# Performance work log

Measured on AMD Instinct MI355X. Metric: run time of the kernel, lower is better.

The kernel has to match this reference:

```python
import jax, jax.numpy as jnp
import numpy as np

N_NODES = 50000
N_EDGES = 400000
H = 64          # node hidden state dim (entities_dimensions['node'])
E_DIM = 8       # edge_params dim (message.extra_parameters)
MSG_HID = 128   # message-creation MLP hidden width
RD_HID = 128    # readout hidden width
T = 2           # message-passing steps


def setup_inputs() -> dict:
    key = jax.random.key(0)
    ks = jax.random.split(key, 12)
    def w(k, shape):
        return jax.random.normal(k, shape, dtype=jnp.float32) * 0.05
    return {
        "node_feats": jax.random.normal(ks[0], (N_NODES, H), dtype=jnp.float32),
        "edge_feats": jax.random.normal(ks[1], (N_EDGES, E_DIM), dtype=jnp.float32),
        "edge_src": jax.random.randint(ks[2], (N_EDGES,), 0, N_NODES),
        "edge_dst": jax.random.randint(ks[3], (N_EDGES,), 0, N_NODES),
        # message creation MLP: concat(hs_src, hs_dst, edge_params) -> relu -> H
        "W_msg1": w(ks[4], (2 * H + E_DIM, MSG_HID)),
        "b_msg1": jnp.zeros((MSG_HID,), jnp.float32),
        "W_msg2": w(ks[5], (MSG_HID, H)),
        "b_msg2": jnp.zeros((H,), jnp.float32),
        # GRU cell update (keras GRUCell convention, reset_after=False)
        "W_x": w(ks[6], (H, 3 * H)),
        "W_h": w(ks[7], (H, 3 * H)),
        "b_gru": jnp.zeros((3 * H,), jnp.float32),
        # readout MLP: H -> relu -> 1
        "W_r1": w(ks[8], (H, RD_HID)),
        "b_r1": jnp.zeros((RD_HID,), jnp.float32),
        "W_r2": w(ks[9], (RD_HID, 1)),
        "b_r2": jnp.zeros((1,), jnp.float32),
    }


def _gru_cell(h, x, W_x, W_h, b):
    # gates order: update (z), reset (r), candidate (h~) — keras convention
    gx = x @ W_x + b
    gh = h @ W_h
    xz, xr, xh = jnp.split(gx, 3, axis=-1)
    hz, hr, hh = jnp.split(gh, 3, axis=-1)
    z = jax.nn.sigmoid(xz + hz)
    r = jax.nn.sigmoid(xr + hr)
    hc = jnp.tanh(xh + r * hh)
    return z * h + (1.0 - z) * hc


def reference(node_feats, edge_feats, edge_src, edge_dst,
              W_msg1, b_msg1, W_msg2, b_msg2,
              W_x, W_h, b_gru, W_r1, b_r1, W_r2, b_r2):
    h = node_feats  # [N, H] hidden states initialized from entity features
    for _ in range(T):
        # gather source/destination node states per edge: [E, H]
        src_h = h[edge_src]
        dst_h = h[edge_dst]
        m_in = jnp.concatenate([src_h, dst_h, edge_feats], axis=-1)  # [E, 2H+E_DIM]
        m = jax.nn.relu(m_in @ W_msg1 + b_msg1) @ W_msg2 + b_msg2    # [E, H]
        # scatter-sum aggregation to destination nodes: [N, H]
        agg = jax.ops.segment_sum(m, edge_dst, num_segments=N_NODES)
        # recurrent (GRU) node-state update
        h = _gru_cell(h, agg, W_x, W_h, b_gru)
    # readout MLP on final hidden states
    out = jax.nn.relu(h @ W_r1 + b_r1) @ W_r2 + b_r2  # [N, 1]
    return out
```

## Files before the change

### kernel.cpp

```cpp
#include <hip/hip_runtime.h>
#include <hip/hip_bf16.h>

#define NN 50000
#define NE 400000
#define NPAIR 12500
#define NCH 196
#define NPAD 50176

typedef __bf16 bf16_t;
typedef __bf16 bf16x4 __attribute__((ext_vector_type(4)));
typedef __bf16 bf16x8 __attribute__((ext_vector_type(8)));
typedef float  floatx4 __attribute__((ext_vector_type(4)));

static __device__ __forceinline__ floatx4 mfma16(bf16x8 a, bf16x8 b, floatx4 c) {
    return __builtin_amdgcn_mfma_f32_16x16x32_bf16(a, b, c, 0, 0, 0);
}
static __device__ __forceinline__ float sigm_f(float x) {
    return 1.f / (1.f + __expf(-x));
}
static __device__ __forceinline__ float tanh_f(float x) {
    return 1.f - 2.f / (__expf(2.f * x) + 1.f);
}
static __device__ __forceinline__ bf16x8 cvt8(const float* sp) {
    float4 f0 = *(const float4*)sp;
    float4 f1 = *(const float4*)(sp + 4);
    bf16x8 v;
    v[0] = (bf16_t)f0.x; v[1] = (bf16_t)f0.y; v[2] = (bf16_t)f0.z; v[3] = (bf16_t)f0.w;
    v[4] = (bf16_t)f1.x; v[5] = (bf16_t)f1.y; v[6] = (bf16_t)f1.z; v[7] = (bf16_t)f1.w;
    return v;
}

__global__ __launch_bounds__(256) void prep_kernel(
    const float* __restrict__ nf,
    const float* __restrict__ Wm1, const float* __restrict__ Wm2,
    const float* __restrict__ Wx,  const float* __restrict__ Wh,
    const float* __restrict__ Wr1,
    bf16_t* __restrict__ hb,
    bf16_t* __restrict__ W1f, bf16_t* __restrict__ W2f,
    bf16_t* __restrict__ Wxt, bf16_t* __restrict__ Wht,
    bf16_t* __restrict__ Wr1f)
{
    int u = blockIdx.x * 256 + threadIdx.x;
    if (u < 800000) {
        float4 v = *(const float4*)(nf + (size_t)u * 4);
        bf16x4 o;
        o[0] = (bf16_t)v.x; o[1] = (bf16_t)v.y; o[2] = (bf16_t)v.z; o[3] = (bf16_t)v.w;
        *(bf16x4*)(hb + (size_t)u * 4) = o;
        return;
    }
    u -= 800000;
    if (u < 20480) {
        int j = u & 7, l = (u >> 3) & 63, rem = u >> 9;
        int ks = rem % 5, nt = rem / 5;
        int n = nt * 16 + (l & 15);
        int k = ks * 32 + (l >> 4) * 8 + j;
        W1f[u] = (k < 136) ? (bf16_t)Wm1[k * 128 + n] : (bf16_t)0.f;
        return;
    }
    u -= 20480;
    if (u < 8192) {
        int j = u & 7, l = (u >> 3) & 63, rem = u >> 9;
        int kg = rem & 3, nt = rem >> 2;
        int n = nt * 16 + (l & 15);
        int k = kg * 32 + (l >> 4) * 8 + j;
        W2f[u] = (bf16_t)Wm2[k * 64 + n];
        return;
    }
    u -= 8192;
    if (u < 12288) {
        int n = u >> 6, k = u & 63;
        Wxt[u] = (bf16_t)Wx[k * 192 + n];
        return;
    }
    u -= 12288;
    if (u < 12288) {
        int n = u >> 6, k = u & 63;
        Wht[u] = (bf16_t)Wh[k * 192 + n];
        return;
    }
    u -= 12288;
    if (u < 8192) {
        int j = u & 7, l = (u >> 3) & 63, rem = u >> 9;
        int kg = rem & 1, nt = rem >> 1;
        int n = nt * 16 + (l & 15);
        int k = kg * 32 + (l >> 4) * 8 + j;
        Wr1f[u] = (bf16_t)Wr1[k * 128 + n];
    }
}

__global__ __launch_bounds__(256) void hist_kernel(
    const int* __restrict__ edst, int* __restrict__ deg)
{
    int e = blockIdx.x * 256 + threadIdx.x;
    if (e < NE) atomicAdd(&deg[edst[e]], 1);
}

__global__ __launch_bounds__(256) void scanA_kernel(
    const int* __restrict__ deg, int* __restrict__ chunkSums)
{
    __shared__ int s[256];
    int i = blockIdx.x * 256 + threadIdx.x;
    s[threadIdx.x] = deg[i];
    __syncthreads();
    for (int st = 128; st >= 1; st >>= 1) {
        if (threadIdx.x < st) s[threadIdx.x] += s[threadIdx.x + st];
        __syncthreads();
    }
    if (threadIdx.x == 0) chunkSums[blockIdx.x] = s[0];
}

__global__ __launch_bounds__(256) void scanB_kernel(
    const int* __restrict__ chunkSums, int* __restrict__ chunkOff)
{
    __shared__ int s[256];
    int t = threadIdx.x;
    int v = (t < NCH) ? chunkSums[t] : 0;
    s[t] = v;
    __syncthreads();
    for (int st = 1; st < 256; st <<= 1) {
        int add = (t >= st) ? s[t - st] : 0;
        __syncthreads();
        s[t] += add;
        __syncthreads();
    }
    if (t < NCH) chunkOff[t] = s[t] - v;
}

__global__ __launch_bounds__(256) void scanC_kernel(
    const int* __restrict__ deg, const int* __restrict__ chunkOff,
    int* __restrict__ cursor)
{
    __shared__ int s[256];
    int t = threadIdx.x;
    int i = blockIdx.x * 256 + t;
    int v = deg[i];
    s[t] = v;
    __syncthreads();
    for (int st = 1; st < 256; st <<= 1) {
        int add = (t >= st) ? s[t - st] : 0;
        __syncthreads();
        s[t] += add;
        __syncthreads();
    }
    cursor[i] = chunkOff[blockIdx.x] + s[t] - v;
}

__global__ __launch_bounds__(256) void scatter_kernel(
    const int* __restrict__ esrc, const int* __restrict__ edst,
    const float* __restrict__ ef,
    int* __restrict__ cursor, int* __restrict__ srcs, int* __restrict__ dsts,
    bf16_t* __restrict__ efpb)
{
    int e = blockIdx.x * 256 + threadIdx.x;
    if (e >= NE) return;
    int d = edst[e];
    int p = atomicAdd(&cursor[d], 1);
    srcs[p] = esrc[e];
    dsts[p] = d;
    float4 a = *(const float4*)(ef + (size_t)e * 8);
    float4 b = *(const float4*)(ef + (size_t)e * 8 + 4);
    bf16x8 v;
    v[0] = (bf16_t)a.x; v[1] = (bf16_t)a.y; v[2] = (bf16_t)a.z; v[3] = (bf16_t)a.w;
    v[4] = (bf16_t)b.x; v[5] = (bf16_t)b.y; v[6] = (bf16_t)b.z; v[7] = (bf16_t)b.w;
    *(bf16x8*)(efpb + (size_t)p * 8) = v;
}

__global__ __launch_bounds__(256) void edge_kernel(
    const bf16_t* __restrict__ hb, const bf16_t* __restrict__ efpb,
    const int* __restrict__ srcs, const int* __restrict__ dsts,
    const bf16_t* __restrict__ W1f, const bf16_t* __restrict__ W2f,
    const float* __restrict__ b1f, const float* __restrict__ b2f,
    float* __restrict__ agg)
{
    __shared__ __attribute__((aligned(16))) bf16_t w1s[20480];
    __shared__ __attribute__((aligned(16))) bf16_t w2s[8192];
    __shared__ __attribute__((aligned(16))) bf16_t hq[4][32 * 36];

    const int tid = threadIdx.x;
    {
        const uint4* s1 = (const uint4*)W1f;
        uint4* d1 = (uint4*)w1s;
        #pragma unroll
        for (int i = 0; i < 10; i++) d1[tid + i * 256] = s1[tid + i * 256];
        const uint4* s2 = (const uint4*)W2f;
        uint4* d2 = (uint4*)w2s;
        #pragma unroll
        for (int i = 0; i < 4; i++) d2[tid + i * 256] = s2[tid + i * 256];
    }
    __syncthreads();

    const int lane = tid & 63;
    const int wv   = tid >> 6;
    const int l15  = lane & 15;
    const int quad = lane >> 4;

    float b1r[8], b2r[4];
    #pragma unroll
    for (int nt = 0; nt < 8; nt++) b1r[nt] = b1f[nt * 16 + l15];
    #pragma unroll
    for (int nt = 0; nt < 4; nt++) b2r[nt] = b2f[nt * 16 + l15];

    const int WTOT = gridDim.x * 4;
    int p = blockIdx.x * 4 + wv;

    bf16x8 af0[5], af1[5];
    int4 d40, d41;
    {
        int base = p * 32;
        int r0 = base + l15, r1 = base + 16 + l15;
        int si0 = srcs[r0], di0 = dsts[r0];
        int si1 = srcs[r1], di1 = dsts[r1];
        const bf16_t* sp0 = hb + (size_t)si0 * 64 + quad * 8;
        const bf16_t* dp0 = hb + (size_t)di0 * 64 + quad * 8;
        const bf16_t* sp1 = hb + (size_t)si1 * 64 + quad * 8;
        const bf16_t* dp1 = hb + (size_t)di1 * 64 + quad * 8;
        af0[0] = *(const bf16x8*)sp0;  af0[1] = *(const bf16x8*)(sp0 + 32);
        af0[2] = *(const bf16x8*)dp0;  af0[3] = *(const bf16x8*)(dp0 + 32);
        af1[0] = *(const bf16x8*)sp1;  af1[1] = *(const bf16x8*)(sp1 + 32);
        af1[2] = *(const bf16x8*)dp1;  af1[3] = *(const bf16x8*)(dp1 + 32);
        if (quad == 0) {
            af0[4] = *(const bf16x8*)(efpb + (size_t)r0 * 8);
            af1[4] = *(const bf16x8*)(efpb + (size_t)r1 * 8);
        } else {
            #pragma unroll
            for (int q = 0; q < 8; q++) { af0[4][q] = (bf16_t)0.f; af1[4][q] = (bf16_t)0.f; }
        }
        d40 = *(const int4*)(dsts + base + quad * 4);
        d41 = *(const int4*)(dsts + base + 16 + quad * 4);
    }

    while (true) {
        int pn = p + WTOT;
        int pp = (pn < NPAIR) ? pn : p;
        int nbase = pp * 32;
        int nr0 = nbase + l15, nr1 = nbase + 16 + l15;
        int si0n = srcs[nr0], di0n = dsts[nr0];
        int si1n = srcs[nr1], di1n = dsts[nr1];
        int4 d40n = *(const int4*)(dsts + nbase + quad * 4);
        int4 d41n = *(const int4*)(dsts + nbase + 16 + quad * 4);

        floatx4 oa0[4], oa1[4];
        #pragma unroll
        for (int nt = 0; nt < 4; nt++) {
            oa0[nt].x=0.f; oa0[nt].y=0.f; oa0[nt].z=0.f; oa0[nt].w=0.f;
            oa1[nt].x=0.f; oa1[nt].y=0.f; oa1[nt].z=0.f; oa1[nt].w=0.f;
        }

        #pragma unroll
        for (int q = 0; q < 4; q++) {
            floatx4 ac0[2], ac1[2];
            #pragma unroll
            for (int nt = 0; nt < 2; nt++) {
                ac0[nt].x=0.f; ac0[nt].y=0.f; ac0[nt].z=0.f; ac0[nt].w=0.f;
                ac1[nt].x=0.f; ac1[nt].y=0.f; ac1[nt].z=0.f; ac1[nt].w=0.f;
            }
            #pragma unroll
            for (int nt = 0; nt < 2; nt++) {
                int gnt = q * 2 + nt;
                #pragma unroll
                for (int ks = 0; ks < 5; ks++) {
                    bf16x8 b = *(const bf16x8*)(w1s + ((gnt * 5 + ks) * 64 + lane) * 8);
                    ac0[nt] = mfma16(af0[ks], b, ac0[nt]);
                    ac1[nt] = mfma16(af1[ks], b, ac1[nt]);
                }
            }
            #pragma unroll
            for (int nt = 0; nt < 2; nt++) {
                float bb = b1r[q * 2 + nt];
                #pragma unroll
                for (int r = 0; r < 4; r++) {
                    float v0 = fmaxf(ac0[nt][r] + bb, 0.f);
                    float v1 = fmaxf(ac1[nt][r] + bb, 0.f);
                    hq[wv][(quad * 4 + r) * 36 + nt * 16 + l15]        = (bf16_t)v0;
                    hq[wv][(16 + quad * 4 + r) * 36 + nt * 16 + l15]   = (bf16_t)v1;
                }
            }
            bf16x8 hf0 = *(const bf16x8*)(hq[wv] + l15 * 36 + quad * 8);
            bf16x8 hf1 = *(const bf16x8*)(hq[wv] + (16 + l15) * 36 + quad * 8);
            #pragma unroll
            for (int nt = 0; nt < 4; nt++) {
                bf16x8 w2 = *(const bf16x8*)(w2s + ((nt * 4 + q) * 64 + lane) * 8);
                oa0[nt] = mfma16(hf0, w2, oa0[nt]);
                oa1[nt] = mfma16(hf1, w2, oa1[nt]);
            }
        }

        {
            const bf16_t* sp0 = hb + (size_t)si0n * 64 + quad * 8;
            const bf16_t* dp0 = hb + (size_t)di0n * 64 + quad * 8;
            const bf16_t* sp1 = hb + (size_t)si1n * 64 + quad * 8;
            const bf16_t* dp1 = hb + (size_t)di1n * 64 + quad * 8;
            af0[0] = *(const bf16x8*)sp0;  af0[1] = *(const bf16x8*)(sp0 + 32);
            af0[2] = *(const bf16x8*)dp0;  af0[3] = *(const bf16x8*)(dp0 + 32);
            af1[0] = *(const bf16x8*)sp1;  af1[1] = *(const bf16x8*)(sp1 + 32);
            af1[2] = *(const bf16x8*)dp1;  af1[3] = *(const bf16x8*)(dp1 + 32);
            if (quad == 0) {
                af0[4] = *(const bf16x8*)(efpb + (size_t)nr0 * 8);
                af1[4] = *(const bf16x8*)(efpb + (size_t)nr1 * 8);
            }
        }

        #pragma unroll
        for (int nt = 0; nt < 4; nt++) {
            int col = nt * 16 + l15;
            float bb = b2r[nt];
            float* ap = agg + col;
            {
                int dcur = d40.x;
                float v = oa0[nt][0] + bb;
                if (d40.y == dcur) v += oa0[nt][1] + bb;
                else { atomicAdd(ap + (size_t)dcur * 64, v); dcur = d40.y; v = oa0[nt][1] + bb; }
                if (d40.z == dcur) v += oa0[nt][2] + bb;
                else { atomicAdd(ap + (size_t)dcur * 64, v); dcur = d40.z; v = oa0[nt][2] + bb; }
                if (d40.w == dcur) v += oa0[nt][3] + bb;
                else { atomicAdd(ap + (size_t)dcur * 64, v); dcur = d40.w; v = oa0[nt][3] + bb; }
                atomicAdd(ap + (size_t)dcur * 64, v);
            }
            {
                int dcur = d41.x;
                float v = oa1[nt][0] + bb;
                if (d41.y == dcur) v += oa1[nt][1] + bb;
                else { atomicAdd(ap + (size_t)dcur * 64, v); dcur = d41.y; v = oa1[nt][1] + bb; }
                if (d41.z == dcur) v += oa1[nt][2] + bb;
                else { atomicAdd(ap + (size_t)dcur * 64, v); dcur = d41.z; v = oa1[nt][2] + bb; }
                if (d41.w == dcur) v += oa1[nt][3] + bb;
                else { atomicAdd(ap + (size_t)dcur * 64, v); dcur = d41.w; v = oa1[nt][3] + bb; }
                atomicAdd(ap + (size_t)dcur * 64, v);
            }
        }

        if (pn >= NPAIR) break;
        p = pn;
        d40 = d40n;
        d41 = d41n;
    }
}

template<int LAST>
__global__ __launch_bounds__(256) void gru_kernel(
    float* __restrict__ agg, const float* __restrict__ h_in,
    float* __restrict__ h_out, bf16_t* __restrict__ hb_out,
    const bf16_t* __restrict__ Wxt, const bf16_t* __restrict__ Wht,
    const float* __restrict__ bg,
    const bf16_t* __restrict__ Wr1f, const float* __restrict__ br1,
    const float* __restrict__ Wr2, const float* __restrict__ br2,
    float* __restrict__ out)
{
    __shared__ __attribute__((aligned(16))) float  shd[64 * 68];
    __shared__ __attribute__((aligned(16))) bf16_t hb2[4][16 * 72];
    const int tid = threadIdx.x;
    const int n0  = blockIdx.x * 64;

    for (int idx = tid; idx < 64 * 16; idx += 256) {
        int i = idx >> 4, c = (idx & 15) * 4;
        int n = n0 + i; if (n >= NN) n = NN - 1;
        *(float4*)&shd[i * 68 + c] = *(const float4*)(h_in + (size_t)n * 64 + c);
    }
    __syncthreads();

    const int lane = tid & 63;
    const int wv   = tid >> 6;
    const int l15  = lane & 15;
    const int quad = lane >> 4;
    const int rowA = wv * 16 + l15;
    const bool rowOK = (n0 + rowA) < NN;
    int nA = n0 + rowA; if (!rowOK) nA = NN - 1;

    bf16x8 ax[2], ah[2];
    ax[0] = cvt8(agg + (size_t)nA * 64 + quad * 8);
    ax[1] = cvt8(agg + (size_t)nA * 64 + quad * 8 + 32);
    {
        const float* hp = shd + rowA * 68 + quad * 8;
        ah[0] = cvt8(hp);
        ah[1] = cvt8(hp + 32);
    }
    if (!LAST && rowOK) {
        float4 z = make_float4(0.f, 0.f, 0.f, 0.f);
        *(float4*)(agg + (size_t)nA * 64 + quad * 8)      = z;
        *(float4*)(agg + (size_t)nA * 64 + quad * 8 + 4)  = z;
        *(float4*)(agg + (size_t)nA * 64 + quad * 8 + 32) = z;
        *(float4*)(agg + (size_t)nA * 64 + quad * 8 + 36) = z;
    }

    floatx4 az[4], ar[4], axh[4], ahh[4];
    #pragma unroll
    for (int nt = 0; nt < 4; nt++) {
        az[nt].x=0.f; az[nt].y=0.f; az[nt].z=0.f; az[nt].w=0.f;
        ar[nt].x=0.f; ar[nt].y=0.f; ar[nt].z=0.f; ar[nt].w=0.f;
        axh[nt].x=0.f; axh[nt].y=0.f; axh[nt].z=0.f; axh[nt].w=0.f;
        ahh[nt].x=0.f; ahh[nt].y=0.f; ahh[nt].z=0.f; ahh[nt].w=0.f;
    }
    #pragma unroll
    for (int nt = 0; nt < 4; nt++) {
        const bf16_t* bx_z = Wxt + (nt * 16 + l15) * 64 + quad * 8;
        const bf16_t* bh_z = Wht + (nt * 16 + l15) * 64 + quad * 8;
        const bf16_t* bx_r = bx_z + 64 * 64;
        const bf16_t* bh_r = bh_z + 64 * 64;
        const bf16_t* bx_h = bx_z + 128 * 64;
        const bf16_t* bh_h = bh_z + 128 * 64;
        az[nt]  = mfma16(ax[0], *(const bf16x8*)bx_z,        az[nt]);
        az[nt]  = mfma16(ax[1], *(const bf16x8*)(bx_z + 32), az[nt]);
        az[nt]  = mfma16(ah[0], *(const bf16x8*)bh_z,        az[nt]);
        az[nt]  = mfma16(ah[1], *(const bf16x8*)(bh_z + 32), az[nt]);
        ar[nt]  = mfma16(ax[0], *(const bf16x8*)bx_r,        ar[nt]);
        ar[nt]  = mfma16(ax[1], *(const bf16x8*)(bx_r + 32), ar[nt]);
        ar[nt]  = mfma16(ah[0], *(const bf16x8*)bh_r,        ar[nt]);
        ar[nt]  = mfma16(ah[1], *(const bf16x8*)(bh_r + 32), ar[nt]);
        axh[nt] = mfma16(ax[0], *(const bf16x8*)bx_h,        axh[nt]);
        axh[nt] = mfma16(ax[1], *(const bf16x8*)(bx_h + 32), axh[nt]);
        ahh[nt] = mfma16(ah[0], *(const bf16x8*)bh_h,        ahh[nt]);
        ahh[nt] = mfma16(ah[1], *(const bf16x8*)(bh_h + 32), ahh[nt]);
    }

    #pragma unroll
    for (int nt = 0; nt < 4; nt++) {
        int j = nt * 16 + l15;
        float bz = bg[j], brr = bg[64 + j], bh = bg[128 + j];
        #pragma unroll
        for (int r = 0; r < 4; r++) {
            int lrow = wv * 16 + quad * 4 + r;
            int n = n0 + lrow;
            float z  = sigm_f(az[nt][r] + bz);
            float rr = sigm_f(ar[nt][r] + brr);
            float hc = tanh_f(axh[nt][r] + bh + rr * ahh[nt][r]);
            float hold = shd[lrow * 68 + j];
            float hnew = z * hold + (1.f - z) * hc;
            if (LAST) {
                hb2[wv][(quad * 4 + r) * 72 + j] = (bf16_t)hnew;
            } else if (n < NN) {
                h_out[(size_t)n * 64 + j]  = hnew;
                hb_out[(size_t)n * 64 + j] = (bf16_t)hnew;
            }
        }
    }

    if (LAST) {
        bf16x8 a0 = *(const bf16x8*)(hb2[wv] + l15 * 72 + quad * 8);
        bf16x8 a1 = *(const bf16x8*)(hb2[wv] + l15 * 72 + quad * 8 + 32);
        floatx4 accR[8];
        #pragma unroll
        for (int nt = 0; nt < 8; nt++) { accR[nt].x=0.f; accR[nt].y=0.f; accR[nt].z=0.f; accR[nt].w=0.f; }
        #pragma unroll
        for (int nt = 0; nt < 8; nt++) {
            bf16x8 b0 = *(const bf16x8*)(Wr1f + ((nt * 2 + 0) * 64 + lane) * 8);
            bf16x8 b1 = *(const bf16x8*)(Wr1f + ((nt * 2 + 1) * 64 + lane) * 8);
            accR[nt] = mfma16(a0, b0, accR[nt]);
            accR[nt] = mfma16(a1, b1, accR[nt]);
        }
        float br1r[8], wr2r[8];
        #pragma unroll
        for (int nt = 0; nt < 8; nt++) {
            br1r[nt] = br1[nt * 16 + l15];
            wr2r[nt] = Wr2[nt * 16 + l15];
        }
        float br2v = br2[0];
        #pragma unroll
        for (int r = 0; r < 4; r++) {
            float p = 0.f;
            #pragma unroll
            for (int nt = 0; nt < 8; nt++)
                p += fmaxf(accR[nt][r] + br1r[nt], 0.f) * wr2r[nt];
            p += __shfl_xor(p, 1, 64);
            p += __shfl_xor(p, 2, 64);
            p += __shfl_xor(p, 4, 64);
            p += __shfl_xor(p, 8, 64);
            if (l15 == 0) {
                int n = n0 + wv * 16 + quad * 4 + r;
                if (n < NN) out[n] = p + br2v;
            }
        }
    }
}

extern "C" void kernel_launch(void* const* d_in, const int* in_sizes, int n_in,
                              void* d_out, int out_size, void* d_ws, size_t ws_size,
                              hipStream_t stream)
{
    const float* nf  = (const float*)d_in[0];
    const float* ef  = (const float*)d_in[1];
    const int* esrc  = (const int*)d_in[2];
    const int* edst  = (const int*)d_in[3];
    const float* Wm1 = (const float*)d_in[4];
    const float* bm1 = (const float*)d_in[5];
    const float* Wm2 = (const float*)d_in[6];
    const float* bm2 = (const float*)d_in[7];
    const float* Wx  = (const float*)d_in[8];
    const float* Wh  = (const float*)d_in[9];
    const float* bg  = (const float*)d_in[10];
    const float* Wr1 = (const float*)d_in[11];
    const float* br1 = (const float*)d_in[12];
    const float* Wr2 = (const float*)d_in[13];
    const float* br2 = (const float*)d_in[14];

    char* ws = (char*)d_ws;
    float*  hbuf   = (float*)(ws);
    bf16_t* hb     = (bf16_t*)(ws + 12800000);
    bf16_t* W1f    = (bf16_t*)(ws + 19200000);
    bf16_t* W2f    = (bf16_t*)(ws + 19240960);
    bf16_t* Wxt    = (bf16_t*)(ws + 19257344);
    bf16_t* Wht    = (bf16_t*)(ws + 19281920);
    bf16_t* Wr1f   = (bf16_t*)(ws + 19306496);
    int*    srcs   = (int*)(ws + 19322880);
    int*    dsts   = (int*)(ws + 20922880);
    bf16_t* efpb   = (bf16_t*)(ws + 22522880);
    int*    deg    = (int*)(ws + 28922880);
    float*  agg    = (float*)(ws + 29123584);
    int*    cursor = (int*)(ws + 41923584);
    int*    chunkS = (int*)(ws + 42124288);
    int*    chunkO = (int*)(ws + 42125312);

    prep_kernel<<<3365, 256, 0, stream>>>(nf, Wm1, Wm2, Wx, Wh, Wr1,
                                          hb, W1f, W2f, Wxt, Wht, Wr1f);

    hipMemsetAsync(deg, 0, (size_t)NPAD * 4 + (size_t)NN * 64 * 4, stream);
    hist_kernel<<<(NE + 255) / 256, 256, 0, stream>>>(edst, deg);
    scanA_kernel<<<NCH, 256, 0, stream>>>(deg, chunkS);
    scanB_kernel<<<1, 256, 0, stream>>>(chunkS, chunkO);
    scanC_kernel<<<NCH, 256, 0, stream>>>(deg, chunkO, cursor);
    scatter_kernel<<<(NE + 255) / 256, 256, 0, stream>>>(esrc, edst, ef, cursor,
                                                         srcs, dsts, efpb);

    edge_kernel<<<1024, 256, 0, stream>>>(hb, efpb, srcs, dsts,
                                          W1f, W2f, bm1, bm2, agg);
    gru_kernel<0><<<(NN + 63) / 64, 256, 0, stream>>>(
        agg, nf, hbuf, hb, Wxt, Wht, bg, Wr1f, br1, Wr2, br2, (float*)d_out);
    edge_kernel<<<1024, 256, 0, stream>>>(hb, efpb, srcs, dsts,
                                          W1f, W2f, bm1, bm2, agg);
    gru_kernel<1><<<(NN + 63) / 64, 256, 0, stream>>>(
        agg, hbuf, nullptr, nullptr, Wxt, Wht, bg, Wr1f, br1, Wr2, br2,
        (float*)d_out);
}
```

Measured before the change: 356.4 us.

## Replace persistent edge loop with one tile per wave, W2 in registers

The edge kernel drops its persistent grid-stride loop with software prefetch of the next tile. It now launches NPAIR/4 blocks, and each wave handles exactly one 32-edge tile. The W2 weights move from shared memory into per-lane registers, which shrinks LDS use per block and may let more blocks fit per CU. In exchange, every block reloads the 40KB W1 slab into LDS and W2 from global memory for a single tile. Cross-iteration prefetch overlap is also lost, and register pressure rises from the 16 extra bf16x8 values.

```diff
diff --git a/kernel.cpp b/kernel.cpp
--- a/kernel.cpp
+++ b/kernel.cpp
@@ -173,7 +173,6 @@
     float* __restrict__ agg)
 {
     __shared__ __attribute__((aligned(16))) bf16_t w1s[20480];
-    __shared__ __attribute__((aligned(16))) bf16_t w2s[8192];
     __shared__ __attribute__((aligned(16))) bf16_t hq[4][32 * 36];
 
     const int tid = threadIdx.x;
@@ -182,32 +181,33 @@
         uint4* d1 = (uint4*)w1s;
         #pragma unroll
         for (int i = 0; i < 10; i++) d1[tid + i * 256] = s1[tid + i * 256];
-        const uint4* s2 = (const uint4*)W2f;
-        uint4* d2 = (uint4*)w2s;
-        #pragma unroll
-        for (int i = 0; i < 4; i++) d2[tid + i * 256] = s2[tid + i * 256];
-    }
-    __syncthreads();
+    }
 
     const int lane = tid & 63;
     const int wv   = tid >> 6;
     const int l15  = lane & 15;
     const int quad = lane >> 4;
 
+    bf16x8 w2f[4][4];
+    #pragma unroll
+    for (int nt = 0; nt < 4; nt++)
+        #pragma unroll
+        for (int kg = 0; kg < 4; kg++)
+            w2f[nt][kg] = *(const bf16x8*)(W2f + ((nt * 4 + kg) * 64 + lane) * 8);
+
     float b1r[8], b2r[4];
     #pragma unroll
     for (int nt = 0; nt < 8; nt++) b1r[nt] = b1f[nt * 16 + l15];
     #pragma unroll
     for (int nt = 0; nt < 4; nt++) b2r[nt] = b2f[nt * 16 + l15];
 
-    const int WTOT = gridDim.x * 4;
-    int p = blockIdx.x * 4 + wv;
+    const int p = blockIdx.x * 4 + wv;
+    const int base = p * 32;
+    const int r0 = base + l15, r1 = base + 16 + l15;
 
     bf16x8 af0[5], af1[5];
     int4 d40, d41;
     {
-        int base = p * 32;
-        int r0 = base + l15, r1 = base + 16 + l15;
         int si0 = srcs[r0], di0 = dsts[r0];
         int si1 = srcs[r1], di1 = dsts[r1];
         const bf16_t* sp0 = hb + (size_t)si0 * 64 + quad * 8;
@@ -228,111 +228,80 @@
         d40 = *(const int4*)(dsts + base + quad * 4);
         d41 = *(const int4*)(dsts + base + 16 + quad * 4);
     }
-
-    while (true) {
-        int pn = p + WTOT;
-        int pp = (pn < NPAIR) ? pn : p;
-        int nbase = pp * 32;
-        int nr0 = nbase + l15, nr1 = nbase + 16 + l15;
-        int si0n = srcs[nr0], di0n = dsts[nr0];
-        int si1n = srcs[nr1], di1n = dsts[nr1];
-        int4 d40n = *(const int4*)(dsts + nbase + quad * 4);
-        int4 d41n = *(const int4*)(dsts + nbase + 16 + quad * 4);
-
-        floatx4 oa0[4], oa1[4];
+    __syncthreads();
+
+    floatx4 oa0[4], oa1[4];
+    #pragma unroll
+    for (int nt = 0; nt < 4; nt++) {
+        oa0[nt].x=0.f; oa0[nt].y=0.f; oa0[nt].z=0.f; oa0[nt].w=0.f;
+        oa1[nt].x=0.f; oa1[nt].y=0.f; oa1[nt].z=0.f; oa1[nt].w=0.f;
+    }
+
+    #pragma unroll
+    for (int q = 0; q < 4; q++) {
+        floatx4 ac0[2], ac1[2];
+        #pragma unroll
+        for (int nt = 0; nt < 2; nt++) {
+            ac0[nt].x=0.f; ac0[nt].y=0.f; ac0[nt].z=0.f; ac0[nt].w=0.f;
+            ac1[nt].x=0.f; ac1[nt].y=0.f; ac1[nt].z=0.f; ac1[nt].w=0.f;
+        }
+        #pragma unroll
+        for (int nt = 0; nt < 2; nt++) {
+            int gnt = q * 2 + nt;
+            #pragma unroll
+            for (int ks = 0; ks < 5; ks++) {
+                bf16x8 b = *(const bf16x8*)(w1s + ((gnt * 5 + ks) * 64 + lane) * 8);
+                ac0[nt] = mfma16(af0[ks], b, ac0[nt]);
+                ac1[nt] = mfma16(af1[ks], b, ac1[nt]);
+            }
+        }
+        #pragma unroll
+        for (int nt = 0; nt < 2; nt++) {
+            float bb = b1r[q * 2 + nt];
+            #pragma unroll
+            for (int r = 0; r < 4; r++) {
+                float v0 = fmaxf(ac0[nt][r] + bb, 0.f);
+                float v1 = fmaxf(ac1[nt][r] + bb, 0.f);
+                hq[wv][(quad * 4 + r) * 36 + nt * 16 + l15]      = (bf16_t)v0;
+                hq[wv][(16 + quad * 4 + r) * 36 + nt * 16 + l15] = (bf16_t)v1;
+            }
+        }
+        bf16x8 hf0 = *(const bf16x8*)(hq[wv] + l15 * 36 + quad * 8);
+        bf16x8 hf1 = *(const bf16x8*)(hq[wv] + (16 + l15) * 36 + quad * 8);
         #pragma unroll
         for (int nt = 0; nt < 4; nt++) {
-            oa0[nt].x=0.f; oa0[nt].y=0.f; oa0[nt].z=0.f; oa0[nt].w=0.f;
-            oa1[nt].x=0.f; oa1[nt].y=0.f; oa1[nt].z=0.f; oa1[nt].w=0.f;
-        }
-
-        #pragma unroll
-        for (int q = 0; q < 4; q++) {
-            floatx4 ac0[2], ac1[2];
-            #pragma unroll
-            for (int nt = 0; nt < 2; nt++) {
-                ac0[nt].x=0.f; ac0[nt].y=0.f; ac0[nt].z=0.f; ac0[nt].w=0.f;
-                ac1[nt].x=0.f; ac1[nt].y=0.f; ac1[nt].z=0.f; ac1[nt].w=0.f;
-            }
-            #pragma unroll
-            for (int nt = 0; nt < 2; nt++) {
-                int gnt = q * 2 + nt;
-                #pragma unroll
-                for (int ks = 0; ks < 5; ks++) {
-                    bf16x8 b = *(const bf16x8*)(w1s + ((gnt * 5 + ks) * 64 + lane) * 8);
-                    ac0[nt] = mfma16(af0[ks], b, ac0[nt]);
-                    ac1[nt] = mfma16(af1[ks], b, ac1[nt]);
-                }
-            }
-            #pragma unroll
-            for (int nt = 0; nt < 2; nt++) {
-                float bb = b1r[q * 2 + nt];
-                #pragma unroll
-                for (int r = 0; r < 4; r++) {
-                    float v0 = fmaxf(ac0[nt][r] + bb, 0.f);
-                    float v1 = fmaxf(ac1[nt][r] + bb, 0.f);
-                    hq[wv][(quad * 4 + r) * 36 + nt * 16 + l15]        = (bf16_t)v0;
-                    hq[wv][(16 + quad * 4 + r) * 36 + nt * 16 + l15]   = (bf16_t)v1;
-                }
-            }
-            bf16x8 hf0 = *(const bf16x8*)(hq[wv] + l15 * 36 + quad * 8);
-            bf16x8 hf1 = *(const bf16x8*)(hq[wv] + (16 + l15) * 36 + quad * 8);
-            #pragma unroll
-            for (int nt = 0; nt < 4; nt++) {
-                bf16x8 w2 = *(const bf16x8*)(w2s + ((nt * 4 + q) * 64 + lane) * 8);
-                oa0[nt] = mfma16(hf0, w2, oa0[nt]);
-                oa1[nt] = mfma16(hf1, w2, oa1[nt]);
-            }
-        }
-
+            oa0[nt] = mfma16(hf0, w2f[nt][q], oa0[nt]);
+            oa1[nt] = mfma16(hf1, w2f[nt][q], oa1[nt]);
+        }
+    }
+
+    #pragma unroll
+    for (int nt = 0; nt < 4; nt++) {
+        int col = nt * 16 + l15;
+        float bb = b2r[nt];
+        float* ap = agg + col;
         {
-            const bf16_t* sp0 = hb + (size_t)si0n * 64 + quad * 8;
-            const bf16_t* dp0 = hb + (size_t)di0n * 64 + quad * 8;
-            const bf16_t* sp1 = hb + (size_t)si1n * 64 + quad * 8;
-            const bf16_t* dp1 = hb + (size_t)di1n * 64 + quad * 8;
-            af0[0] = *(const bf16x8*)sp0;  af0[1] = *(const bf16x8*)(sp0 + 32);
-            af0[2] = *(const bf16x8*)dp0;  af0[3] = *(const bf16x8*)(dp0 + 32);
-            af1[0] = *(const bf16x8*)sp1;  af1[1] = *(const bf16x8*)(sp1 + 32);
-            af1[2] = *(const bf16x8*)dp1;  af1[3] = *(const bf16x8*)(dp1 + 32);
-            if (quad == 0) {
-                af0[4] = *(const bf16x8*)(efpb + (size_t)nr0 * 8);
-                af1[4] = *(const bf16x8*)(efpb + (size_t)nr1 * 8);
-            }
-        }
-
-        #pragma unroll
-        for (int nt = 0; nt < 4; nt++) {
-            int col = nt * 16 + l15;
-            float bb = b2r[nt];
-            float* ap = agg + col;
-            {
-                int dcur = d40.x;
-                float v = oa0[nt][0] + bb;
-                if (d40.y == dcur) v += oa0[nt][1] + bb;
-                else { atomicAdd(ap + (size_t)dcur * 64, v); dcur = d40.y; v = oa0[nt][1] + bb; }
-                if (d40.z == dcur) v += oa0[nt][2] + bb;
-                else { atomicAdd(ap + (size_t)dcur * 64, v); dcur = d40.z; v = oa0[nt][2] + bb; }
-                if (d40.w == dcur) v += oa0[nt][3] + bb;
-                else { atomicAdd(ap + (size_t)dcur * 64, v); dcur = d40.w; v = oa0[nt][3] + bb; }
-                atomicAdd(ap + (size_t)dcur * 64, v);
-            }
-            {
-                int dcur = d41.x;
-                float v = oa1[nt][0] + bb;
-                if (d41.y == dcur) v += oa1[nt][1] + bb;
-                else { atomicAdd(ap + (size_t)dcur * 64, v); dcur = d41.y; v = oa1[nt][1] + bb; }
-                if (d41.z == dcur) v += oa1[nt][2] + bb;
-                else { atomicAdd(ap + (size_t)dcur * 64, v); dcur = d41.z; v = oa1[nt][2] + bb; }
-                if (d41.w == dcur) v += oa1[nt][3] + bb;
-                else { atomicAdd(ap + (size_t)dcur * 64, v); dcur = d41.w; v = oa1[nt][3] + bb; }
-                atomicAdd(ap + (size_t)dcur * 64, v);
-            }
-        }
-
-        if (pn >= NPAIR) break;
-        p = pn;
-        d40 = d40n;
-        d41 = d41n;
+            int dcur = d40.x;
+            float v = oa0[nt][0] + bb;
+            if (d40.y == dcur) v += oa0[nt][1] + bb;
+            else { atomicAdd(ap + (size_t)dcur * 64, v); dcur = d40.y; v = oa0[nt][1] + bb; }
+            if (d40.z == dcur) v += oa0[nt][2] + bb;
+            else { atomicAdd(ap + (size_t)dcur * 64, v); dcur = d40.z; v = oa0[nt][2] + bb; }
+            if (d40.w == dcur) v += oa0[nt][3] + bb;
+            else { atomicAdd(ap + (size_t)dcur * 64, v); dcur = d40.w; v = oa0[nt][3] + bb; }
+            atomicAdd(ap + (size_t)dcur * 64, v);
+        }
+        {
+            int dcur = d41.x;
+            float v = oa1[nt][0] + bb;
+            if (d41.y == dcur) v += oa1[nt][1] + bb;
+            else { atomicAdd(ap + (size_t)dcur * 64, v); dcur = d41.y; v = oa1[nt][1] + bb; }
+            if (d41.z == dcur) v += oa1[nt][2] + bb;
+            else { atomicAdd(ap + (size_t)dcur * 64, v); dcur = d41.z; v = oa1[nt][2] + bb; }
+            if (d41.w == dcur) v += oa1[nt][3] + bb;
+            else { atomicAdd(ap + (size_t)dcur * 64, v); dcur = d41.w; v = oa1[nt][3] + bb; }
+            atomicAdd(ap + (size_t)dcur * 64, v);
+        }
     }
 }
 
@@ -520,12 +489,12 @@
     scatter_kernel<<<(NE + 255) / 256, 256, 0, stream>>>(esrc, edst, ef, cursor,
                                                          srcs, dsts, efpb);
 
-    edge_kernel<<<1024, 256, 0, stream>>>(hb, efpb, srcs, dsts,
-                                          W1f, W2f, bm1, bm2, agg);
+    edge_kernel<<<NPAIR / 4, 256, 0, stream>>>(hb, efpb, srcs, dsts,
+                                               W1f, W2f, bm1, bm2, agg);
     gru_kernel<0><<<(NN + 63) / 64, 256, 0, stream>>>(
         agg, nf, hbuf, hb, Wxt, Wht, bg, Wr1f, br1, Wr2, br2, (float*)d_out);
-    edge_kernel<<<1024, 256, 0, stream>>>(hb, efpb, srcs, dsts,
-                                          W1f, W2f, bm1, bm2, agg);
+    edge_kernel<<<NPAIR / 4, 256, 0, stream>>>(hb, efpb, srcs, dsts,
+                                               W1f, W2f, bm1, bm2, agg);
     gru_kernel<1><<<(NN + 63) / 64, 256, 0, stream>>>(
         agg, hbuf, nullptr, nullptr, Wxt, Wht, bg, Wr1f, br1, Wr2, br2,
         (float*)d_out);
```

Result: slower. 371.4 us (+4.2%).

## Replace atomic scatter-add with bf16 message buffer and CSR segmented reduction

Applied to the files above, without the earlier changes.

The edge kernel no longer does float atomicAdds into a per-node aggregate. It now writes each edge's message as bf16 into a dense buffer in destination-sorted order. A new agg_kernel then sums each node's contiguous edge range, using the degree and the scanned cursor, into a bf16 aggregate. The GRU kernel reads this bf16 aggregate and no longer zeroes it, and the large memset goes away. In exchange there is an extra 51 MB write and read of messages per step plus an extra launch, and rounding to bf16 twice loses some precision.

```diff
diff --git a/kernel.cpp b/kernel.cpp
--- a/kernel.cpp
+++ b/kernel.cpp
@@ -170,7 +170,7 @@
     const int* __restrict__ srcs, const int* __restrict__ dsts,
     const bf16_t* __restrict__ W1f, const bf16_t* __restrict__ W2f,
     const float* __restrict__ b1f, const float* __restrict__ b2f,
-    float* __restrict__ agg)
+    bf16_t* __restrict__ mb)
 {
     __shared__ __attribute__((aligned(16))) bf16_t w1s[20480];
     __shared__ __attribute__((aligned(16))) bf16_t w2s[8192];
@@ -204,7 +204,6 @@
     int p = blockIdx.x * 4 + wv;
 
     bf16x8 af0[5], af1[5];
-    int4 d40, d41;
     {
         int base = p * 32;
         int r0 = base + l15, r1 = base + 16 + l15;
@@ -225,8 +224,6 @@
             #pragma unroll
             for (int q = 0; q < 8; q++) { af0[4][q] = (bf16_t)0.f; af1[4][q] = (bf16_t)0.f; }
         }
-        d40 = *(const int4*)(dsts + base + quad * 4);
-        d41 = *(const int4*)(dsts + base + 16 + quad * 4);
     }
 
     while (true) {
@@ -236,8 +233,6 @@
         int nr0 = nbase + l15, nr1 = nbase + 16 + l15;
         int si0n = srcs[nr0], di0n = dsts[nr0];
         int si1n = srcs[nr1], di1n = dsts[nr1];
-        int4 d40n = *(const int4*)(dsts + nbase + quad * 4);
-        int4 d41n = *(const int4*)(dsts + nbase + 16 + quad * 4);
 
         floatx4 oa0[4], oa1[4];
         #pragma unroll
@@ -271,8 +266,8 @@
                 for (int r = 0; r < 4; r++) {
                     float v0 = fmaxf(ac0[nt][r] + bb, 0.f);
                     float v1 = fmaxf(ac1[nt][r] + bb, 0.f);
-                    hq[wv][(quad * 4 + r) * 36 + nt * 16 + l15]        = (bf16_t)v0;
-                    hq[wv][(16 + quad * 4 + r) * 36 + nt * 16 + l15]   = (bf16_t)v1;
+                    hq[wv][(quad * 4 + r) * 36 + nt * 16 + l15]      = (bf16_t)v0;
+                    hq[wv][(16 + quad * 4 + r) * 36 + nt * 16 + l15] = (bf16_t)v1;
                 }
             }
             bf16x8 hf0 = *(const bf16x8*)(hq[wv] + l15 * 36 + quad * 8);
@@ -285,6 +280,7 @@
             }
         }
 
+        int base = p * 32;
         {
             const bf16_t* sp0 = hb + (size_t)si0n * 64 + quad * 8;
             const bf16_t* dp0 = hb + (size_t)di0n * 64 + quad * 8;
@@ -304,41 +300,43 @@
         for (int nt = 0; nt < 4; nt++) {
             int col = nt * 16 + l15;
             float bb = b2r[nt];
-            float* ap = agg + col;
-            {
-                int dcur = d40.x;
-                float v = oa0[nt][0] + bb;
-                if (d40.y == dcur) v += oa0[nt][1] + bb;
-                else { atomicAdd(ap + (size_t)dcur * 64, v); dcur = d40.y; v = oa0[nt][1] + bb; }
-                if (d40.z == dcur) v += oa0[nt][2] + bb;
-                else { atomicAdd(ap + (size_t)dcur * 64, v); dcur = d40.z; v = oa0[nt][2] + bb; }
-                if (d40.w == dcur) v += oa0[nt][3] + bb;
-                else { atomicAdd(ap + (size_t)dcur * 64, v); dcur = d40.w; v = oa0[nt][3] + bb; }
-                atomicAdd(ap + (size_t)dcur * 64, v);
-            }
-            {
-                int dcur = d41.x;
-                float v = oa1[nt][0] + bb;
-                if (d41.y == dcur) v += oa1[nt][1] + bb;
-                else { atomicAdd(ap + (size_t)dcur * 64, v); dcur = d41.y; v = oa1[nt][1] + bb; }
-                if (d41.z == dcur) v += oa1[nt][2] + bb;
-                else { atomicAdd(ap + (size_t)dcur * 64, v); dcur = d41.z; v = oa1[nt][2] + bb; }
-                if (d41.w == dcur) v += oa1[nt][3] + bb;
-                else { atomicAdd(ap + (size_t)dcur * 64, v); dcur = d41.w; v = oa1[nt][3] + bb; }
-                atomicAdd(ap + (size_t)dcur * 64, v);
+            #pragma unroll
+            for (int r = 0; r < 4; r++) {
+                int row0 = base + quad * 4 + r;
+                int row1 = base + 16 + quad * 4 + r;
+                mb[(size_t)row0 * 64 + col] = (bf16_t)(oa0[nt][r] + bb);
+                mb[(size_t)row1 * 64 + col] = (bf16_t)(oa1[nt][r] + bb);
             }
         }
 
         if (pn >= NPAIR) break;
         p = pn;
-        d40 = d40n;
-        d41 = d41n;
-    }
+    }
+}
+
+__global__ __launch_bounds__(256) void agg_kernel(
+    const bf16_t* __restrict__ mb, const int* __restrict__ deg,
+    const int* __restrict__ cursor, bf16_t* __restrict__ aggb)
+{
+    const int node = blockIdx.x * 4 + (threadIdx.x >> 6);
+    if (node >= NN) return;
+    const int lane = threadIdx.x & 63;
+    int dg  = deg[node];
+    int end = cursor[node];
+    int st  = end - dg;
+    float s0 = 0.f, s1 = 0.f;
+    int e = st;
+    for (; e + 1 < end; e += 2) {
+        s0 += (float)mb[(size_t)e * 64 + lane];
+        s1 += (float)mb[(size_t)(e + 1) * 64 + lane];
+    }
+    if (e < end) s0 += (float)mb[(size_t)e * 64 + lane];
+    aggb[(size_t)node * 64 + lane] = (bf16_t)(s0 + s1);
 }
 
 template<int LAST>
 __global__ __launch_bounds__(256) void gru_kernel(
-    float* __restrict__ agg, const float* __restrict__ h_in,
+    const bf16_t* __restrict__ aggb, const float* __restrict__ h_in,
     float* __restrict__ h_out, bf16_t* __restrict__ hb_out,
     const bf16_t* __restrict__ Wxt, const bf16_t* __restrict__ Wht,
     const float* __restrict__ bg,
@@ -363,23 +361,15 @@
     const int l15  = lane & 15;
     const int quad = lane >> 4;
     const int rowA = wv * 16 + l15;
-    const bool rowOK = (n0 + rowA) < NN;
-    int nA = n0 + rowA; if (!rowOK) nA = NN - 1;
+    int nA = n0 + rowA; if (nA >= NN) nA = NN - 1;
 
     bf16x8 ax[2], ah[2];
-    ax[0] = cvt8(agg + (size_t)nA * 64 + quad * 8);
-    ax[1] = cvt8(agg + (size_t)nA * 64 + quad * 8 + 32);
+    ax[0] = *(const bf16x8*)(aggb + (size_t)nA * 64 + quad * 8);
+    ax[1] = *(const bf16x8*)(aggb + (size_t)nA * 64 + quad * 8 + 32);
     {
         const float* hp = shd + rowA * 68 + quad * 8;
         ah[0] = cvt8(hp);
         ah[1] = cvt8(hp + 32);
-    }
-    if (!LAST && rowOK) {
-        float4 z = make_float4(0.f, 0.f, 0.f, 0.f);
-        *(float4*)(agg + (size_t)nA * 64 + quad * 8)      = z;
-        *(float4*)(agg + (size_t)nA * 64 + quad * 8 + 4)  = z;
-        *(float4*)(agg + (size_t)nA * 64 + quad * 8 + 32) = z;
-        *(float4*)(agg + (size_t)nA * 64 + quad * 8 + 36) = z;
     }
 
     floatx4 az[4], ar[4], axh[4], ahh[4];
@@ -504,15 +494,16 @@
     int*    dsts   = (int*)(ws + 20922880);
     bf16_t* efpb   = (bf16_t*)(ws + 22522880);
     int*    deg    = (int*)(ws + 28922880);
-    float*  agg    = (float*)(ws + 29123584);
-    int*    cursor = (int*)(ws + 41923584);
-    int*    chunkS = (int*)(ws + 42124288);
-    int*    chunkO = (int*)(ws + 42125312);
+    int*    cursor = (int*)(ws + 29123584);
+    int*    chunkS = (int*)(ws + 29324288);
+    int*    chunkO = (int*)(ws + 29325312);
+    bf16_t* aggb   = (bf16_t*)(ws + 29326336);
+    bf16_t* mb     = (bf16_t*)(ws + 35726336);
 
     prep_kernel<<<3365, 256, 0, stream>>>(nf, Wm1, Wm2, Wx, Wh, Wr1,
                                           hb, W1f, W2f, Wxt, Wht, Wr1f);
 
-    hipMemsetAsync(deg, 0, (size_t)NPAD * 4 + (size_t)NN * 64 * 4, stream);
+    hipMemsetAsync(deg, 0, (size_t)NPAD * 4, stream);
     hist_kernel<<<(NE + 255) / 256, 256, 0, stream>>>(edst, deg);
     scanA_kernel<<<NCH, 256, 0, stream>>>(deg, chunkS);
     scanB_kernel<<<1, 256, 0, stream>>>(chunkS, chunkO);
@@ -521,12 +512,14 @@
                                                          srcs, dsts, efpb);
 
     edge_kernel<<<1024, 256, 0, stream>>>(hb, efpb, srcs, dsts,
-                                          W1f, W2f, bm1, bm2, agg);
+                                          W1f, W2f, bm1, bm2, mb);
+    agg_kernel<<<(NN + 3) / 4, 256, 0, stream>>>(mb, deg, cursor, aggb);
     gru_kernel<0><<<(NN + 63) / 64, 256, 0, stream>>>(
-        agg, nf, hbuf, hb, Wxt, Wht, bg, Wr1f, br1, Wr2, br2, (float*)d_out);
+        aggb, nf, hbuf, hb, Wxt, Wht, bg, Wr1f, br1, Wr2, br2, (float*)d_out);
     edge_kernel<<<1024, 256, 0, stream>>>(hb, efpb, srcs, dsts,
-                                          W1f, W2f, bm1, bm2, agg);
+                                          W1f, W2f, bm1, bm2, mb);
+    agg_kernel<<<(NN + 3) / 4, 256, 0, stream>>>(mb, deg, cursor, aggb);
     gru_kernel<1><<<(NN + 63) / 64, 256, 0, stream>>>(
-        agg, hbuf, nullptr, nullptr, Wxt, Wht, bg, Wr1f, br1, Wr2, br2,
+        aggb, hbuf, nullptr, nullptr, Wxt, Wht, bg, Wr1f, br1, Wr2, br2,
         (float*)d_out);
 }
```

After: 322.8 us. 9.4% less time.
